# Performance work log

Hardware: AMD Instinct MI355X
Metric: run time of the kernel (lower is better)

Reference implementation:

```python
import jax, jax.numpy as jnp
import numpy as np

B, L, DIM = 16, 131072, 9  # batch, audio samples, 1 fundamental + 8 harmonics
SR = 22050.0
SINE_AMP = 0.1
NOISE_STD = 0.003


def setup_inputs() -> dict:
    key = jax.random.key(0)
    k1, k2, k3, k4 = jax.random.split(key, 4)
    u = jax.random.uniform(k1, (B, L, 1), dtype=jnp.float32)
    voiced = jax.random.uniform(k2, (B, L, 1), dtype=jnp.float32) > 0.3
    f0 = jnp.where(voiced, 100.0 + 300.0 * u, 0.0)  # Hz, 0 where unvoiced
    rand_ini = jax.random.uniform(k3, (B, DIM), dtype=jnp.float32)
    rand_ini = rand_ini.at[:, 0].set(0.0)  # first harmonic gets no random phase
    noise_z = jax.random.normal(k4, (B, L, DIM), dtype=jnp.float32)
    return {"f0": f0, "rand_ini": rand_ini, "noise_z": noise_z}


def reference(f0, rand_ini, noise_z):
    dim = noise_z.shape[-1]
    two_pi = 2.0 * jnp.pi
    # harmonic multiples of f0: (B, L, dim)
    k = jnp.arange(1, dim + 1, dtype=f0.dtype)
    fn = f0 * k
    # normalized per-step phase increment in [0, 1)
    rad = jnp.mod(fn / SR, 1.0)
    rad = rad.at[:, 0, :].add(rand_ini)  # random initial phase per harmonic
    # wrap-around detection: cumulative phase mod 1 decreases at a wrap
    tmp_over_one = jnp.mod(jnp.cumsum(rad, axis=1), 1.0)
    wrap = (tmp_over_one[:, 1:, :] - tmp_over_one[:, :-1, :]) < 0.0
    cumsum_shift = jnp.concatenate(
        [jnp.zeros_like(rad[:, :1, :]), jnp.where(wrap, -1.0, 0.0).astype(rad.dtype)],
        axis=1,
    )
    sines = jnp.sin(jnp.cumsum(rad + cumsum_shift, axis=1) * two_pi)
    sine_waves = sines * SINE_AMP
    # voiced/unvoiced mask from fundamental f0
    uv = (f0 > 0.0).astype(f0.dtype)  # (B, L, 1)
    noise_amp = uv * NOISE_STD + (1.0 - uv) * (SINE_AMP / 3.0)
    noise = noise_amp * noise_z
    sine_waves = sine_waves * uv + noise
    return sine_waves, uv, noise
```

## Files before the change

### kernel.cpp

```cpp
#include <hip/hip_runtime.h>
#include <math.h>


#define Bq 16
#define Lq 131072
#define DIMq 9
#define CHUNK 1024
#define NCHUNK (Lq / CHUNK)
#define NPBLK (Bq * NCHUNK)
#define BT 2048
#define NMBLK (Bq * (Lq / BT))
#define NT 256
#define NT2 512
#define PT 4
#define Q4 (BT * DIMq / 4 / NT2)

typedef float f32x4 __attribute__((ext_vector_type(4)));
typedef float f32x2 __attribute__((ext_vector_type(2)));
typedef double f64x2 __attribute__((ext_vector_type(2)));

__global__ void __launch_bounds__(NT, 8) k_partials(
    const float* __restrict__ f0, double* __restrict__ part) {
  int bc = blockIdx.x;
  int b = bc >> 7, c = bc & 127;
  int tid = threadIdx.x, lane = tid & 63, wave = tid >> 6;
  const f32x4* p = (const f32x4*)(f0 + (size_t)b * Lq + (size_t)c * CHUNK);
  f32x4 x = p[tid];
  double s = ((double)x.x + (double)x.y) + ((double)x.z + (double)x.w);
#pragma unroll
  for (int d = 32; d > 0; d >>= 1) s += __shfl_xor(s, d, 64);
  __shared__ double ws[NT / 64];
  if (lane == 0) ws[wave] = s;
  __syncthreads();
  if (tid == 0) part[bc] = (ws[0] + ws[1]) + (ws[2] + ws[3]);
}

__global__ void __launch_bounds__(NT2, 8) k_main(
    const float* __restrict__ f0, const float* __restrict__ rini,
    const float* __restrict__ nz, const double* __restrict__ part,
    float* __restrict__ out0, float* __restrict__ out1,
    float* __restrict__ out2) {
  int bc = blockIdx.x;
  int b = bc >> 6, cp = bc & 63;
  int tid = threadIdx.x, lane = tid & 63, wave = tid >> 6;
  size_t t0g = (size_t)b * Lq + (size_t)cp * BT;

  __shared__ f32x2 ps[BT];
  __shared__ double wsum[NT2 / 64];

  f32x4 fa = *(const f32x4*)(f0 + t0g + tid * PT);
  float fv[PT] = {fa.x, fa.y, fa.z, fa.w};
  double run = 0.0, inc[PT];
#pragma unroll
  for (int j = 0; j < PT; ++j) { run += (double)fv[j]; inc[j] = run; }
  double tot = run;
#pragma unroll
  for (int d = 1; d < 64; d <<= 1) {
    double o = __shfl_up(tot, d, 64);
    if (lane >= d) tot += o;
  }
  if (lane == 63) wsum[wave] = tot;
  __syncthreads();

  f64x2 pp = ((const f64x2*)(part + (b << 7)))[lane];
  double pv = (lane < cp) ? (pp.x + pp.y) : 0.0;
#pragma unroll
  for (int d = 32; d > 0; d >>= 1) pv += __shfl_xor(pv, d, 64);
  double wpre = 0.0;
  for (int w = 0; w < wave; ++w) wpre += wsum[w];
  double base = pv + wpre + (tot - run);

  const double invsr = 1.0 / 22050.0;
  const float nampU = (float)(0.1 / 3.0);
  float uvv[PT];
#pragma unroll
  for (int j = 0; j < PT; ++j) {
    double ph = __builtin_amdgcn_fract((base + inc[j]) * invsr);
    bool v = fv[j] > 0.0f;
    f32x2 e = {(float)ph, v ? 0.003f : -nampU};
    ps[tid * PT + j] = e;
    uvv[j] = v ? 1.0f : 0.0f;
  }
  f32x4 u0 = {uvv[0], uvv[1], uvv[2], uvv[3]};
  __builtin_nontemporal_store(u0, (f32x4*)(out1 + t0g + tid * PT));

  float inir[DIMq];
#pragma unroll
  for (int d = 0; d < DIMq; ++d) inir[d] = rini[b * DIMq + d];
  __syncthreads();

  const f32x4* nzc = (const f32x4*)(nz + t0g * DIMq);
  f32x4* o0c = (f32x4*)(out0 + t0g * DIMq);
  f32x4* o2c = (f32x4*)(out2 + t0g * DIMq);

  struct R { float r0, r2; };
  auto gen = [&](int t, int d, float nzv) -> R {
    f32x2 e = ps[t];
    float ph = __builtin_amdgcn_fractf((float)(d + 1) * e.x + inir[d]);
    float s = __builtin_amdgcn_sinf(ph) * 0.1f;
    float noise = fabsf(e.y) * nzv;
    R r;
    r.r2 = noise;
    r.r0 = (e.y > 0.0f) ? s + noise : noise;
    return r;
  };

#pragma unroll 3
  for (int w = 0; w < Q4; ++w) {
    int q = w * NT2 + tid;
    int e = q * 4;
    int t = (int)(((unsigned)e * 7282u) >> 16);
    int d = e - t * 9;
    f32x4 nzv = nzc[q];
    R a = gen(t, d, nzv.x); if (++d == 9) { d = 0; ++t; }
    R bb = gen(t, d, nzv.y); if (++d == 9) { d = 0; ++t; }
    R cc = gen(t, d, nzv.z); if (++d == 9) { d = 0; ++t; }
    R dd = gen(t, d, nzv.w);
    f32x4 r0 = {a.r0, bb.r0, cc.r0, dd.r0};
    f32x4 r2 = {a.r2, bb.r2, cc.r2, dd.r2};
    __builtin_nontemporal_store(r0, &o0c[q]);
    __builtin_nontemporal_store(r2, &o2c[q]);
  }
}

extern "C" void kernel_launch(void* const* d_in, const int* in_sizes, int n_in,
                              void* d_out, int out_size, void* d_ws, size_t ws_size,
                              hipStream_t stream) {
  const float* f0 = (const float*)d_in[0];
  const float* rini = (const float*)d_in[1];
  const float* nz = (const float*)d_in[2];
  float* out = (float*)d_out;
  float* out0 = out;
  float* out1 = out + (size_t)Bq * Lq * DIMq;
  float* out2 = out1 + (size_t)Bq * Lq;
  double* part = (double*)d_ws;

  k_partials<<<NPBLK, NT, 0, stream>>>(f0, part);
  k_main<<<NMBLK, NT2, 0, stream>>>(f0, rini, nz, part, out0, out1, out2);
}
```

Baseline: 47.13 us.

## Shrink main tiles to 1024 samples, wave-level partials, prefetch noise loads

The main kernel now uses 256-thread blocks over 1024-sample chunks, which doubles the block count. Each block sums its prefix from per-chunk partials. The partials kernel assigns one wavefront per chunk, with four loads per lane and no shared memory or barrier. The noise loop is software-pipelined with unroll 1 and a one-iteration-ahead prefetch of the noise vector, replacing compiler unrolling. The goal is more parallelism and latency hiding, at the cost of fewer bytes in flight per thread and more blocks doing the prefix setup.

```diff
diff --git a/kernel.cpp b/kernel.cpp
--- a/kernel.cpp
+++ b/kernel.cpp
@@ -7,13 +7,10 @@
 #define DIMq 9
 #define CHUNK 1024
 #define NCHUNK (Lq / CHUNK)
-#define NPBLK (Bq * NCHUNK)
-#define BT 2048
-#define NMBLK (Bq * (Lq / BT))
+#define NBLK (Bq * NCHUNK)
 #define NT 256
-#define NT2 512
 #define PT 4
-#define Q4 (BT * DIMq / 4 / NT2)
+#define Q4 (CHUNK * DIMq / 4 / NT)
 
 typedef float f32x4 __attribute__((ext_vector_type(4)));
 typedef float f32x2 __attribute__((ext_vector_type(2)));
@@ -21,32 +18,31 @@
 
 __global__ void __launch_bounds__(NT, 8) k_partials(
     const float* __restrict__ f0, double* __restrict__ part) {
-  int bc = blockIdx.x;
-  int b = bc >> 7, c = bc & 127;
-  int tid = threadIdx.x, lane = tid & 63, wave = tid >> 6;
-  const f32x4* p = (const f32x4*)(f0 + (size_t)b * Lq + (size_t)c * CHUNK);
-  f32x4 x = p[tid];
-  double s = ((double)x.x + (double)x.y) + ((double)x.z + (double)x.w);
+  int gw = blockIdx.x * (NT / 64) + (threadIdx.x >> 6);
+  int lane = threadIdx.x & 63;
+  const f32x4* p = (const f32x4*)(f0 + (size_t)gw * CHUNK);
+  f32x4 x0 = p[lane], x1 = p[lane + 64], x2 = p[lane + 128], x3 = p[lane + 192];
+  double s = (((double)x0.x + (double)x0.y) + ((double)x0.z + (double)x0.w)) +
+             (((double)x1.x + (double)x1.y) + ((double)x1.z + (double)x1.w)) +
+             (((double)x2.x + (double)x2.y) + ((double)x2.z + (double)x2.w)) +
+             (((double)x3.x + (double)x3.y) + ((double)x3.z + (double)x3.w));
 #pragma unroll
   for (int d = 32; d > 0; d >>= 1) s += __shfl_xor(s, d, 64);
-  __shared__ double ws[NT / 64];
-  if (lane == 0) ws[wave] = s;
-  __syncthreads();
-  if (tid == 0) part[bc] = (ws[0] + ws[1]) + (ws[2] + ws[3]);
+  if (lane == 0) part[gw] = s;
 }
 
-__global__ void __launch_bounds__(NT2, 8) k_main(
+__global__ void __launch_bounds__(NT, 8) k_main(
     const float* __restrict__ f0, const float* __restrict__ rini,
     const float* __restrict__ nz, const double* __restrict__ part,
     float* __restrict__ out0, float* __restrict__ out1,
     float* __restrict__ out2) {
   int bc = blockIdx.x;
-  int b = bc >> 6, cp = bc & 63;
+  int b = bc >> 7, c = bc & 127;
   int tid = threadIdx.x, lane = tid & 63, wave = tid >> 6;
-  size_t t0g = (size_t)b * Lq + (size_t)cp * BT;
+  size_t t0g = (size_t)b * Lq + (size_t)c * CHUNK;
 
-  __shared__ f32x2 ps[BT];
-  __shared__ double wsum[NT2 / 64];
+  __shared__ f32x2 ps[CHUNK];
+  __shared__ double wsum[NT / 64];
 
   f32x4 fa = *(const f32x4*)(f0 + t0g + tid * PT);
   float fv[PT] = {fa.x, fa.y, fa.z, fa.w};
@@ -63,7 +59,7 @@
   __syncthreads();
 
   f64x2 pp = ((const f64x2*)(part + (b << 7)))[lane];
-  double pv = (lane < cp) ? (pp.x + pp.y) : 0.0;
+  double pv = ((2 * lane < c) ? pp.x : 0.0) + ((2 * lane + 1 < c) ? pp.y : 0.0);
 #pragma unroll
   for (int d = 32; d > 0; d >>= 1) pv += __shfl_xor(pv, d, 64);
   double wpre = 0.0;
@@ -105,13 +101,15 @@
     return r;
   };
 
-#pragma unroll 3
+  f32x4 nzv = nzc[tid];
+#pragma unroll 1
   for (int w = 0; w < Q4; ++w) {
-    int q = w * NT2 + tid;
+    int q = w * NT + tid;
+    f32x4 nznext;
+    if (w + 1 < Q4) nznext = nzc[q + NT];
     int e = q * 4;
     int t = (int)(((unsigned)e * 7282u) >> 16);
     int d = e - t * 9;
-    f32x4 nzv = nzc[q];
     R a = gen(t, d, nzv.x); if (++d == 9) { d = 0; ++t; }
     R bb = gen(t, d, nzv.y); if (++d == 9) { d = 0; ++t; }
     R cc = gen(t, d, nzv.z); if (++d == 9) { d = 0; ++t; }
@@ -120,6 +118,7 @@
     f32x4 r2 = {a.r2, bb.r2, cc.r2, dd.r2};
     __builtin_nontemporal_store(r0, &o0c[q]);
     __builtin_nontemporal_store(r2, &o2c[q]);
+    nzv = nznext;
   }
 }
 
@@ -135,6 +134,6 @@
   float* out2 = out1 + (size_t)Bq * Lq;
   double* part = (double*)d_ws;
 
-  k_partials<<<NPBLK, NT, 0, stream>>>(f0, part);
-  k_main<<<NMBLK, NT2, 0, stream>>>(f0, rini, nz, part, out0, out1, out2);
+  k_partials<<<NBLK / (NT / 64), NT, 0, stream>>>(f0, part);
+  k_main<<<NBLK, NT, 0, stream>>>(f0, rini, nz, part, out0, out1, out2);
 }
```

Result: no change. 46.89 us (-0.5%).
